# Performance work log

Hardware: AMD Instinct MI355X
Metric: run time of the kernel (lower is better)

## Reference

```python
import jax, jax.numpy as jnp
import numpy as np

D_MODEL = 1024
NUM_HEADS = 16
THETA = 10000.0
NEG = -1000000.0  # masked_fill value used by the torch code


def _rope(x, token_positions, theta):
    # x: [B, H, S, d_head]; token_positions: [S] int
    d_k = x.shape[-1]
    half = d_k // 2
    j = jnp.arange(half, dtype=jnp.float32)
    inv_freq = theta ** (-(2.0 * j) / d_k)                      # [half]
    ang = token_positions.astype(jnp.float32)[:, None] * inv_freq  # [S, half]
    cos = jnp.cos(ang)
    sin = jnp.sin(ang)
    xp = x.reshape(x.shape[:-1] + (half, 2))  # adjacent pairs (pc, 2)
    x0, x1 = xp[..., 0], xp[..., 1]
    o0 = x0 * cos - x1 * sin
    o1 = x0 * sin + x1 * cos
    out = jnp.stack([o0, o1], axis=-1)
    return out.reshape(x.shape)


def setup_inputs() -> dict:
    key = jax.random.key(0)
    k0, k1, k2 = jax.random.split(key, 3)
    B, S, D = 2, 2048, D_MODEL
    std = (2.0 / (D + D)) ** 0.5
    X = jax.random.normal(k0, (B, S, D), dtype=jnp.float32)
    QKV_weights = jax.random.normal(k1, (3 * D, D), dtype=jnp.float32) * std
    O_weights = jax.random.normal(k2, (D, D), dtype=jnp.float32) * std
    token_positions = jnp.arange(S, dtype=jnp.int32)
    return {"X": X, "token_positions": token_positions,
            "QKV_weights": QKV_weights, "O_weights": O_weights}


def reference(X, token_positions, QKV_weights, O_weights):
    B, S, D = X.shape
    H = NUM_HEADS
    dh = D // H
    qkv = jnp.einsum('od,bsd->bso', QKV_weights, X)  # [B, S, 3D]
    Q, K, V = jnp.split(qkv, 3, axis=-1)

    def split_heads(t):
        return t.reshape(B, S, H, dh).transpose(0, 2, 1, 3)  # [B,H,S,dh]

    Q, K, V = split_heads(Q), split_heads(K), split_heads(V)
    Q = _rope(Q, token_positions, THETA)
    K = _rope(K, token_positions, THETA)

    scores = (jnp.einsum('bhqd,bhkd->bhqk', Q, K) / jnp.sqrt(jnp.float32(dh))).astype(jnp.float32)
    causal = jnp.tril(jnp.ones((S, S), dtype=bool))
    scores = jnp.where(causal, scores, NEG)
    probs = jax.nn.softmax(scores, axis=-1)
    attn = jnp.einsum('bhqk,bhkd->bhqd', probs, V.astype(jnp.float32)).astype(Q.dtype)
    attn = attn.transpose(0, 2, 1, 3).reshape(B, S, D)
    return jnp.einsum('od,bsd->bso', O_weights, attn)
```

## Files before the change

### kernel.cpp

```cpp
#include <hip/hip_runtime.h>
#include <math.h>

#define S_LEN 2048

using bf16x8  = __attribute__((ext_vector_type(8))) short;
using shortx4 = __attribute__((ext_vector_type(4))) short;
using f32x4   = __attribute__((ext_vector_type(4))) float;
using uintx4  = __attribute__((ext_vector_type(4))) unsigned;
using uintx2  = __attribute__((ext_vector_type(2))) unsigned;

static __device__ __forceinline__ short f2bf(float f) {
  unsigned u = __float_as_uint(f);
  u += 0x7fffu + ((u >> 16) & 1u);
  return (short)(u >> 16);
}

#if __has_builtin(__builtin_amdgcn_cvt_pk_bf16_f32)
using bf16x2_t = __attribute__((ext_vector_type(2))) __bf16;
static __device__ __forceinline__ unsigned pkbf(float a, float b) {
  bf16x2_t v = __builtin_amdgcn_cvt_pk_bf16_f32(a, b);
  return __builtin_bit_cast(unsigned, v);
}
#else
static __device__ __forceinline__ unsigned pkbf(float a, float b) {
  return (unsigned)(unsigned short)f2bf(a) | ((unsigned)(unsigned short)f2bf(b) << 16);
}
#endif

#define GLD_LDS16(gptr, lptr)                                                  \
  __builtin_amdgcn_global_load_lds(                                            \
      (__attribute__((address_space(1))) void*)(gptr),                         \
      (__attribute__((address_space(3))) void*)(lptr), 16, 0, 0)

#define EXP2_SHIFT 20.0f

static __device__ __forceinline__ f32x4 exp2s4(f32x4 a) {
  return (f32x4){__builtin_amdgcn_exp2f(a[0] - EXP2_SHIFT),
                 __builtin_amdgcn_exp2f(a[1] - EXP2_SHIFT),
                 __builtin_amdgcn_exp2f(a[2] - EXP2_SHIFT),
                 __builtin_amdgcn_exp2f(a[3] - EXP2_SHIFT)};
}

static __device__ __forceinline__ int sigma64(int k) {
  return (k & 0x20) | ((k & 0x0C) << 1) | ((k & 0x10) >> 2) | (k & 3);
}

__global__ __launch_bounds__(256) void init_kernel(const float* __restrict__ X,
                                                   const float* __restrict__ W1,
                                                   const float* __restrict__ W2,
                                                   const int* __restrict__ tok,
                                                   short* __restrict__ Xb,
                                                   short* __restrict__ W1b,
                                                   short* __restrict__ W2b,
                                                   float2* __restrict__ table) {
  if (blockIdx.x < 4096) {
    size_t idx = (size_t)(blockIdx.x * 256 + threadIdx.x) * 8;
    const float* src;
    short* dst;
    size_t off;
    if (idx < 4194304) { src = X; dst = Xb; off = idx; }
    else if (idx < 4194304 + 3145728) { src = W1; dst = W1b; off = idx - 4194304; }
    else { src = W2; dst = W2b; off = idx - (4194304 + 3145728); }
    float4 a = *(const float4*)(src + off);
    float4 b = *(const float4*)(src + off + 4);
    bf16x8 o = {f2bf(a.x), f2bf(a.y), f2bf(a.z), f2bf(a.w),
                f2bf(b.x), f2bf(b.y), f2bf(b.z), f2bf(b.w)};
    *(bf16x8*)(dst + off) = o;
  } else {
    int i = (blockIdx.x - 4096) * 256 + threadIdx.x;
    int s = i >> 5, j = i & 31;
    double pos = (double)tok[s];
    double ang = pos * pow(10000.0, -(double)j / 32.0);
    table[i] = make_float2((float)cos(ang), (float)sin(ang));
  }
}

template <int BM, typename OutT, int EPI>
__global__ __launch_bounds__(256) void gemm_ll(const short* __restrict__ A,
                                               const short* __restrict__ B,
                                               OutT* __restrict__ C,
                                               const float2* __restrict__ tab,
                                               short* __restrict__ Qb,
                                               short* __restrict__ Kb,
                                               short* __restrict__ VT,
                                               int M, int N, int K) {
  constexpr int MI = BM / 32;
  constexpr int AI = BM / 64;
  __shared__ short As[BM * 32];
  __shared__ short Bs[128 * 32];
  const int tid  = threadIdx.x;
  const int lane = tid & 63;
  const int wv   = tid >> 6;
  const int wm   = (wv >> 1) * (BM / 2);
  const int wn   = (wv & 1) * 64;
  const int m16  = lane & 15;
  const int q4   = lane >> 4;

  const int nwg = gridDim.x * gridDim.y;
  int bid = blockIdx.y * gridDim.x + blockIdx.x;
  bid = (bid & 7) * (nwg >> 3) + (bid >> 3);
  const int rowBase = (bid / gridDim.x) * BM;
  const int colBase = (bid % gridDim.x) * 128;

  const int lrow = lane >> 2;
  const int lchk = (lane & 3) ^ ((lane >> 3) & 3);
  const int fsw  = (q4 ^ ((m16 >> 1) & 3)) * 8;

  f32x4 acc[MI][4];
#pragma unroll
  for (int i = 0; i < MI; ++i)
#pragma unroll
    for (int j = 0; j < 4; ++j) acc[i][j] = (f32x4){0.f, 0.f, 0.f, 0.f};

  const short* Agl = A + (size_t)rowBase * K;
  const short* Bgl = B + (size_t)colBase * K;

  for (int kk = 0; kk < K; kk += 32) {
#pragma unroll
    for (int i = 0; i < AI; ++i) {
      const int r0 = (wv * AI + i) * 16;
      GLD_LDS16(Agl + (size_t)(r0 + lrow) * K + kk + lchk * 8, &As[r0 * 32]);
    }
#pragma unroll
    for (int i = 0; i < 2; ++i) {
      const int r0 = (wv * 2 + i) * 16;
      GLD_LDS16(Bgl + (size_t)(r0 + lrow) * K + kk + lchk * 8, &Bs[r0 * 32]);
    }
    __syncthreads();

    bf16x8 af[MI], bfv[4];
#pragma unroll
    for (int mi = 0; mi < MI; ++mi)
      af[mi] = *(const bf16x8*)&As[(wm + mi * 16 + m16) * 32 + fsw];
#pragma unroll
    for (int ni = 0; ni < 4; ++ni)
      bfv[ni] = *(const bf16x8*)&Bs[(wn + ni * 16 + m16) * 32 + fsw];
#pragma unroll
    for (int mi = 0; mi < MI; ++mi)
#pragma unroll
      for (int ni = 0; ni < 4; ++ni)
        acc[mi][ni] = __builtin_amdgcn_mfma_f32_16x16x32_bf16(af[mi], bfv[ni], acc[mi][ni], 0, 0, 0);
    __syncthreads();
  }

  if constexpr (EPI == 0) {
#pragma unroll
    for (int mi = 0; mi < MI; ++mi)
#pragma unroll
      for (int ni = 0; ni < 4; ++ni) {
        const int rbase = rowBase + wm + mi * 16 + q4 * 4;
        const int cidx  = colBase + wn + ni * 16 + m16;
#pragma unroll
        for (int r = 0; r < 4; ++r) {
          float v = acc[mi][ni][r];
          if constexpr (sizeof(OutT) == 2)
            C[(size_t)(rbase + r) * N + cidx] = (OutT)f2bf(v);
          else
            C[(size_t)(rbase + r) * N + cidx] = (OutT)v;
        }
      }
  } else {
    const int sect = colBase >> 10;
#pragma unroll
    for (int mi = 0; mi < MI; ++mi)
#pragma unroll
      for (int ni = 0; ni < 4; ++ni) {
        const int col = colBase + wn + ni * 16 + m16;
        const int rb  = rowBase + wm + mi * 16 + q4 * 4;
        if (sect == 2) {
          const int hd = col - 2048;
          const int h = hd >> 6, d = hd & 63;
          const int b = rb >> 11, s0 = rb & (S_LEN - 1);
          shortx4 pk4 = {f2bf(acc[mi][ni][0]), f2bf(acc[mi][ni][1]),
                         f2bf(acc[mi][ni][2]), f2bf(acc[mi][ni][3])};
          *(shortx4*)(VT + ((size_t)((b * 16 + h) * 64 + d)) * S_LEN +
                      (s0 & ~63) + sigma64(s0 & 63)) = pk4;
        } else {
          const int cc = col & 1023;
          const int h = cc >> 6, d = cc & 63, j = d >> 1;
          const float sgn = (m16 & 1) ? 1.f : -1.f;
          short* dstp = (sect == 0) ? Qb : Kb;
          const float scl = (sect == 0) ? (0.125f * 1.44269504f) : 1.f;
#pragma unroll
          for (int r = 0; r < 4; ++r) {
            const int row = rb + r;
            const int s = row & (S_LEN - 1), bidx = row >> 11;
            float2 cs = tab[s * 32 + j];
            float self = acc[mi][ni][r];
            float part = __shfl_xor(self, 1);
            float o = (self * cs.x + sgn * part * cs.y) * scl;
            dstp[((size_t)((bidx * 16 + h) * S_LEN + s)) * 64 + d] = f2bf(o);
          }
        }
      }
  }
}

__global__ __launch_bounds__(256, 2) void attn_mfma(const short* __restrict__ Qb,
                                                    const short* __restrict__ Kb,
                                                    const short* __restrict__ VT,
                                                    short* __restrict__ attnb) {
  __shared__ __align__(16) short Smem[9216];
  short* Ks = Smem;
  short* Vs = Smem + 64 * 72;
  const int tid  = threadIdx.x;
  const int lane = tid & 63;
  const int w    = tid >> 6;
  const int m16  = lane & 15;
  const int q4   = lane >> 4;
  const int bh   = blockIdx.x;
  const int jtx  = blockIdx.y;
  const int jt   = (jtx < 8) ? (15 - jtx) : (jtx - 8);
  const int b    = bh >> 4, h = bh & 15;
  const short* Qh = Qb + (size_t)bh * S_LEN * 64;
  const short* Kh = Kb + (size_t)bh * S_LEN * 64;
  const short* Vh = VT + (size_t)bh * 64 * S_LEN;

  const int srow = tid >> 3;
  const int seg  = tid & 7;

  const bf16x8 ones = {16256, 16256, 16256, 16256, 16256, 16256, 16256, 16256};

  const int q0 = jt * 128;
  const int ktiles = 2 * jt + 2;

  bf16x8 qf[2][2];
#pragma unroll
  for (int n = 0; n < 2; ++n)
#pragma unroll
    for (int ks = 0; ks < 2; ++ks)
      qf[n][ks] = *(const bf16x8*)(Qh + (size_t)(q0 + w * 32 + n * 16 + m16) * 64 + ks * 32 + q4 * 8);

  f32x4 O[2][4], Lacc[2];
#pragma unroll
  for (int n = 0; n < 2; ++n) {
    Lacc[n] = (f32x4){0.f, 0.f, 0.f, 0.f};
#pragma unroll
    for (int c = 0; c < 4; ++c) O[n][c] = (f32x4){0.f, 0.f, 0.f, 0.f};
  }

  bf16x8 kst[2], vst[2];
#pragma unroll
  for (int i = 0; i < 2; ++i) {
    kst[i] = *(const bf16x8*)(Kh + (size_t)(i * 32 + srow) * 64 + seg * 8);
    vst[i] = *(const bf16x8*)(Vh + (size_t)(i * 32 + srow) * S_LEN + seg * 8);
  }

  for (int t = 0; t < ktiles; ++t) {
#pragma unroll
    for (int i = 0; i < 2; ++i) {
      *(bf16x8*)&Ks[(i * 32 + srow) * 72 + seg * 8] = kst[i];
      *(bf16x8*)&Vs[(i * 32 + srow) * 72 + seg * 8] = vst[i];
    }
    __syncthreads();

    if (t + 1 < ktiles) {
#pragma unroll
      for (int i = 0; i < 2; ++i) {
        kst[i] = *(const bf16x8*)(Kh + (size_t)((t + 1) * 64 + i * 32 + srow) * 64 + seg * 8);
        vst[i] = *(const bf16x8*)(Vh + (size_t)(i * 32 + srow) * S_LEN + (t + 1) * 64 + seg * 8);
      }
    }

    f32x4 sc[2][4];
#pragma unroll
    for (int n = 0; n < 2; ++n)
#pragma unroll
      for (int c = 0; c < 4; ++c) sc[n][c] = (f32x4){0.f, 0.f, 0.f, 0.f};
#pragma unroll
    for (int ks = 0; ks < 2; ++ks) {
#pragma unroll
      for (int c = 0; c < 4; ++c) {
        bf16x8 kf = *(const bf16x8*)&Ks[(c * 16 + m16) * 72 + ks * 32 + q4 * 8];
#pragma unroll
        for (int n = 0; n < 2; ++n)
          sc[n][c] = __builtin_amdgcn_mfma_f32_16x16x32_bf16(kf, qf[n][ks], sc[n][c], 0, 0, 0);
      }
    }

    if (t >= ktiles - 2) {
#pragma unroll
      for (int n = 0; n < 2; ++n)
#pragma unroll
        for (int c = 0; c < 4; ++c) {
          const int qg = q0 + w * 32 + n * 16 + m16;
#pragma unroll
          for (int rr = 0; rr < 4; ++rr) {
            const int kg = t * 64 + c * 16 + q4 * 4 + rr;
            if (kg > qg) sc[n][c][rr] = -1e30f;
          }
        }
    }

    bf16x8 pb[2][2];
#pragma unroll
    for (int n = 0; n < 2; ++n) {
#pragma unroll
      for (int c = 0; c < 4; ++c) sc[n][c] = exp2s4(sc[n][c]);
      uintx4 u0 = {pkbf(sc[n][0][0], sc[n][0][1]), pkbf(sc[n][0][2], sc[n][0][3]),
                   pkbf(sc[n][1][0], sc[n][1][1]), pkbf(sc[n][1][2], sc[n][1][3])};
      uintx4 u1 = {pkbf(sc[n][2][0], sc[n][2][1]), pkbf(sc[n][2][2], sc[n][2][3]),
                   pkbf(sc[n][3][0], sc[n][3][1]), pkbf(sc[n][3][2], sc[n][3][3])};
      pb[n][0] = __builtin_bit_cast(bf16x8, u0);
      pb[n][1] = __builtin_bit_cast(bf16x8, u1);
    }

#pragma unroll
    for (int ch = 0; ch < 2; ++ch) {
#pragma unroll
      for (int c2 = 0; c2 < 4; ++c2) {
        bf16x8 va = *(const bf16x8*)&Vs[(c2 * 16 + m16) * 72 + ch * 32 + q4 * 8];
#pragma unroll
        for (int n = 0; n < 2; ++n)
          O[n][c2] = __builtin_amdgcn_mfma_f32_16x16x32_bf16(va, pb[n][ch], O[n][c2], 0, 0, 0);
      }
#pragma unroll
      for (int n = 0; n < 2; ++n)
        Lacc[n] = __builtin_amdgcn_mfma_f32_16x16x32_bf16(ones, pb[n][ch], Lacc[n], 0, 0, 0);
    }
    __syncthreads();
  }

#pragma unroll
  for (int n = 0; n < 2; ++n) {
    const float inv = __frcp_rn(Lacc[n][0]);
#pragma unroll
    for (int c2 = 0; c2 < 4; ++c2) {
      uintx2 uo = {pkbf(O[n][c2][0] * inv, O[n][c2][1] * inv),
                   pkbf(O[n][c2][2] * inv, O[n][c2][3] * inv)};
      *(shortx4*)&Smem[(w * 32 + n * 16 + m16) * 72 + c2 * 16 + q4 * 4] =
          __builtin_bit_cast(shortx4, uo);
    }
  }
  __syncthreads();
  {
    const int row = tid >> 1, hf = tid & 1;
    const short* src = &Smem[row * 72 + hf * 32];
    short* dst = attnb + (size_t)(b * S_LEN + q0 + row) * 1024 + h * 64 + hf * 32;
    ((bf16x8*)dst)[0] = ((const bf16x8*)src)[0];
    ((bf16x8*)dst)[1] = ((const bf16x8*)src)[1];
    ((bf16x8*)dst)[2] = ((const bf16x8*)src)[2];
    ((bf16x8*)dst)[3] = ((const bf16x8*)src)[3];
  }
}

extern "C" void kernel_launch(void* const* d_in, const int* in_sizes, int n_in,
                              void* d_out, int out_size, void* d_ws, size_t ws_size,
                              hipStream_t stream) {
  const float* X    = (const float*)d_in[0];
  const int*   tok  = (const int*)d_in[1];
  const float* Wqkv = (const float*)d_in[2];
  const float* Wo   = (const float*)d_in[3];
  float* out = (float*)d_out;

  char* w = (char*)d_ws;
  float2* table = (float2*)w;
  short*  Qb    = (short*)(w + 524288);
  short*  Kb    = Qb + 4194304;
  short*  VTt   = Kb + 4194304;
  short*  Xb    = VTt + 2 * 4194304;
  short*  Wqkvb = Xb + 4194304;
  short*  Wob   = Wqkvb + 3145728;
  short*  attnb = Wob + 1048576;

  hipLaunchKernelGGL(init_kernel, dim3(4352), dim3(256), 0, stream,
                     X, Wqkv, Wo, tok, Xb, Wqkvb, Wob, table);
  hipLaunchKernelGGL((gemm_ll<128, short, 1>), dim3(24, 32), dim3(256), 0, stream,
                     Xb, Wqkvb, (short*)nullptr, table, Qb, Kb, VTt, 4096, 3072, 1024);
  hipLaunchKernelGGL(attn_mfma, dim3(32, 16), dim3(256), 0, stream,
                     Qb, Kb, VTt, attnb);
  hipLaunchKernelGGL((gemm_ll<128, float, 0>), dim3(8, 32), dim3(256), 0, stream,
                     attnb, Wob, out, (const float2*)nullptr,
                     (short*)nullptr, (short*)nullptr, (short*)nullptr,
                     4096, 1024, 1024);
}
```

Measured before the change: 184.3 us.

## Widen GEMM K-tile to 64 with new LDS swizzle; add MFMA setprio in attention

The projection GEMM now stages 64-wide K slices into LDS instead of 32, using an 8-row XOR swizzle for loads and fragment reads, and runs two MFMA k-steps per barrier pair. This halves the number of barrier rounds and global-to-LDS issue phases per output tile, at the cost of doubling LDS use per block. Separately, the attention kernel raises wave priority around its MFMA sections so matrix work is favoured over other waves' memory and exp work.

```diff
diff --git a/kernel.cpp b/kernel.cpp
--- a/kernel.cpp
+++ b/kernel.cpp
@@ -85,9 +85,9 @@
                                                short* __restrict__ VT,
                                                int M, int N, int K) {
   constexpr int MI = BM / 32;
-  constexpr int AI = BM / 64;
-  __shared__ short As[BM * 32];
-  __shared__ short Bs[128 * 32];
+  constexpr int AG = BM / 32;
+  __shared__ short As[BM * 64];
+  __shared__ short Bs[128 * 64];
   const int tid  = threadIdx.x;
   const int lane = tid & 63;
   const int wv   = tid >> 6;
@@ -102,9 +102,10 @@
   const int rowBase = (bid / gridDim.x) * BM;
   const int colBase = (bid % gridDim.x) * 128;
 
-  const int lrow = lane >> 2;
-  const int lchk = (lane & 3) ^ ((lane >> 3) & 3);
-  const int fsw  = (q4 ^ ((m16 >> 1) & 3)) * 8;
+  const int r8 = lane >> 3;
+  const int sl = lane & 7;
+  const int ssw = (sl ^ r8) * 8;
+  const int fx  = (m16 & 7);
 
   f32x4 acc[MI][4];
 #pragma unroll
@@ -115,31 +116,35 @@
   const short* Agl = A + (size_t)rowBase * K;
   const short* Bgl = B + (size_t)colBase * K;
 
-  for (int kk = 0; kk < K; kk += 32) {
-#pragma unroll
-    for (int i = 0; i < AI; ++i) {
-      const int r0 = (wv * AI + i) * 16;
-      GLD_LDS16(Agl + (size_t)(r0 + lrow) * K + kk + lchk * 8, &As[r0 * 32]);
-    }
-#pragma unroll
-    for (int i = 0; i < 2; ++i) {
-      const int r0 = (wv * 2 + i) * 16;
-      GLD_LDS16(Bgl + (size_t)(r0 + lrow) * K + kk + lchk * 8, &Bs[r0 * 32]);
+  for (int kk = 0; kk < K; kk += 64) {
+#pragma unroll
+    for (int i = 0; i < AG; ++i) {
+      const int g = wv * AG + i;
+      GLD_LDS16(Agl + (size_t)(g * 8 + r8) * K + kk + ssw, &As[g * 512]);
+    }
+#pragma unroll
+    for (int i = 0; i < 4; ++i) {
+      const int g = wv * 4 + i;
+      GLD_LDS16(Bgl + (size_t)(g * 8 + r8) * K + kk + ssw, &Bs[g * 512]);
     }
     __syncthreads();
 
-    bf16x8 af[MI], bfv[4];
-#pragma unroll
-    for (int mi = 0; mi < MI; ++mi)
-      af[mi] = *(const bf16x8*)&As[(wm + mi * 16 + m16) * 32 + fsw];
-#pragma unroll
-    for (int ni = 0; ni < 4; ++ni)
-      bfv[ni] = *(const bf16x8*)&Bs[(wn + ni * 16 + m16) * 32 + fsw];
-#pragma unroll
-    for (int mi = 0; mi < MI; ++mi)
+#pragma unroll
+    for (int ks = 0; ks < 2; ++ks) {
+      const int fo = ((ks * 4 + q4) ^ fx) * 8;
+      bf16x8 af[MI], bfv[4];
 #pragma unroll
       for (int ni = 0; ni < 4; ++ni)
-        acc[mi][ni] = __builtin_amdgcn_mfma_f32_16x16x32_bf16(af[mi], bfv[ni], acc[mi][ni], 0, 0, 0);
+        bfv[ni] = *(const bf16x8*)&Bs[(wn + ni * 16 + m16) * 64 + fo];
+#pragma unroll
+      for (int mi = 0; mi < MI; ++mi)
+        af[mi] = *(const bf16x8*)&As[(wm + mi * 16 + m16) * 64 + fo];
+#pragma unroll
+      for (int mi = 0; mi < MI; ++mi)
+#pragma unroll
+        for (int ni = 0; ni < 4; ++ni)
+          acc[mi][ni] = __builtin_amdgcn_mfma_f32_16x16x32_bf16(af[mi], bfv[ni], acc[mi][ni], 0, 0, 0);
+    }
     __syncthreads();
   }
 
@@ -267,6 +272,7 @@
     for (int n = 0; n < 2; ++n)
 #pragma unroll
       for (int c = 0; c < 4; ++c) sc[n][c] = (f32x4){0.f, 0.f, 0.f, 0.f};
+    __builtin_amdgcn_s_setprio(1);
 #pragma unroll
     for (int ks = 0; ks < 2; ++ks) {
 #pragma unroll
@@ -277,6 +283,7 @@
           sc[n][c] = __builtin_amdgcn_mfma_f32_16x16x32_bf16(kf, qf[n][ks], sc[n][c], 0, 0, 0);
       }
     }
+    __builtin_amdgcn_s_setprio(0);
 
     if (t >= ktiles - 2) {
 #pragma unroll
@@ -305,6 +312,7 @@
       pb[n][1] = __builtin_bit_cast(bf16x8, u1);
     }
 
+    __builtin_amdgcn_s_setprio(1);
 #pragma unroll
     for (int ch = 0; ch < 2; ++ch) {
 #pragma unroll
@@ -318,6 +326,7 @@
       for (int n = 0; n < 2; ++n)
         Lacc[n] = __builtin_amdgcn_mfma_f32_16x16x32_bf16(ones, pb[n][ch], Lacc[n], 0, 0, 0);
     }
+    __builtin_amdgcn_s_setprio(0);
     __syncthreads();
   }
 
```

Measured after the change: 189.8 us. 3.0% more time.

## Stage full-K weight panel in LDS and stream A fragments from global

Applied to the files above, without the earlier changes.

Replaces the k-looped tiled GEMM with a kernel that loads a whole 64-column by 1024-K weight panel (128 KB) into swizzled LDS once. Each wave then reads its A fragments directly from global memory with double-buffered registers, so the main loop has no block barriers. This removes per-k-step synchronisation and LDS staging of A, at the cost of very high LDS use (one block per CU) and uncached-in-LDS A reads that depend on L2/L1 reuse. Separately, the attention kernel raises wave priority around its MFMA sections.

```diff
diff --git a/kernel.cpp b/kernel.cpp
--- a/kernel.cpp
+++ b/kernel.cpp
@@ -75,98 +75,99 @@
   }
 }
 
-template <int BM, typename OutT, int EPI>
-__global__ __launch_bounds__(256) void gemm_ll(const short* __restrict__ A,
-                                               const short* __restrict__ B,
-                                               OutT* __restrict__ C,
+template <int EPI>
+__global__ __launch_bounds__(512) void gemm_bs(const short* __restrict__ A,
+                                               const short* __restrict__ Bw,
+                                               float* __restrict__ C,
                                                const float2* __restrict__ tab,
                                                short* __restrict__ Qb,
                                                short* __restrict__ Kb,
-                                               short* __restrict__ VT,
-                                               int M, int N, int K) {
-  constexpr int MI = BM / 32;
-  constexpr int AI = BM / 64;
-  __shared__ short As[BM * 32];
-  __shared__ short Bs[128 * 32];
+                                               short* __restrict__ VT) {
+  __shared__ short Bs[65536];
   const int tid  = threadIdx.x;
   const int lane = tid & 63;
   const int wv   = tid >> 6;
-  const int wm   = (wv >> 1) * (BM / 2);
-  const int wn   = (wv & 1) * 64;
   const int m16  = lane & 15;
   const int q4   = lane >> 4;
 
-  const int nwg = gridDim.x * gridDim.y;
-  int bid = blockIdx.y * gridDim.x + blockIdx.x;
-  bid = (bid & 7) * (nwg >> 3) + (bid >> 3);
-  const int rowBase = (bid / gridDim.x) * BM;
-  const int colBase = (bid % gridDim.x) * 128;
-
-  const int lrow = lane >> 2;
-  const int lchk = (lane & 3) ^ ((lane >> 3) & 3);
-  const int fsw  = (q4 ^ ((m16 >> 1) & 3)) * 8;
-
-  f32x4 acc[MI][4];
-#pragma unroll
-  for (int i = 0; i < MI; ++i)
+  const int bid = blockIdx.x;
+  const int mtg = bid & 15;
+  const int ntb = bid >> 4;
+
+  {
+    const short* Bgl = Bw + (size_t)ntb * 64 * 1024;
+    const int u = tid >> 7;
+    const int slot = tid & 127;
+#pragma unroll
+    for (int j = 0; j < 16; ++j) {
+      const int r = j * 4 + u;
+      const int gs = slot ^ (r & 7);
+      GLD_LDS16(Bgl + (size_t)r * 1024 + gs * 8, &Bs[j * 4096 + tid * 8]);
+    }
+  }
+  __syncthreads();
+
+  const int mtb = mtg * 256 + wv * 32;
+  const short* Aw = A + (size_t)(mtb + m16) * 1024 + q4 * 8;
+  const int bsw = (m16 & 7);
+
+  f32x4 acc[2][4];
+#pragma unroll
+  for (int i = 0; i < 2; ++i)
 #pragma unroll
     for (int j = 0; j < 4; ++j) acc[i][j] = (f32x4){0.f, 0.f, 0.f, 0.f};
 
-  const short* Agl = A + (size_t)rowBase * K;
-  const short* Bgl = B + (size_t)colBase * K;
-
-  for (int kk = 0; kk < K; kk += 32) {
-#pragma unroll
-    for (int i = 0; i < AI; ++i) {
-      const int r0 = (wv * AI + i) * 16;
-      GLD_LDS16(Agl + (size_t)(r0 + lrow) * K + kk + lchk * 8, &As[r0 * 32]);
-    }
-#pragma unroll
-    for (int i = 0; i < 2; ++i) {
-      const int r0 = (wv * 2 + i) * 16;
-      GLD_LDS16(Bgl + (size_t)(r0 + lrow) * K + kk + lchk * 8, &Bs[r0 * 32]);
-    }
-    __syncthreads();
-
-    bf16x8 af[MI], bfv[4];
-#pragma unroll
-    for (int mi = 0; mi < MI; ++mi)
-      af[mi] = *(const bf16x8*)&As[(wm + mi * 16 + m16) * 32 + fsw];
-#pragma unroll
-    for (int ni = 0; ni < 4; ++ni)
-      bfv[ni] = *(const bf16x8*)&Bs[(wn + ni * 16 + m16) * 32 + fsw];
-#pragma unroll
-    for (int mi = 0; mi < MI; ++mi)
-#pragma unroll
-      for (int ni = 0; ni < 4; ++ni)
-        acc[mi][ni] = __builtin_amdgcn_mfma_f32_16x16x32_bf16(af[mi], bfv[ni], acc[mi][ni], 0, 0, 0);
-    __syncthreads();
-  }
+#define LDA(t, mi) (*(const bf16x8*)(Aw + (size_t)(mi) * 16384 + (size_t)(t) * 32))
+#define STEP(t, aX)                                                            \
+  do {                                                                         \
+    bf16x8 bfv[4];                                                             \
+    _Pragma("unroll")                                                          \
+    for (int ni = 0; ni < 4; ++ni)                                             \
+      bfv[ni] = *(const bf16x8*)&Bs[(ni * 16 + m16) * 1024 +                   \
+                                    (((t) * 4 + q4) ^ bsw) * 8];               \
+    _Pragma("unroll")                                                          \
+    for (int mi = 0; mi < 2; ++mi)                                             \
+      _Pragma("unroll")                                                        \
+      for (int ni = 0; ni < 4; ++ni)                                           \
+        acc[mi][ni] = __builtin_amdgcn_mfma_f32_16x16x32_bf16(                 \
+            aX[mi], bfv[ni], acc[mi][ni], 0, 0, 0);                            \
+  } while (0)
+
+  bf16x8 aE[2], aO[2];
+#pragma unroll
+  for (int mi = 0; mi < 2; ++mi) aE[mi] = LDA(0, mi);
+  for (int t = 0; t < 32; t += 2) {
+#pragma unroll
+    for (int mi = 0; mi < 2; ++mi) aO[mi] = LDA(t + 1, mi);
+    STEP(t, aE);
+    if (t + 2 < 32) {
+#pragma unroll
+      for (int mi = 0; mi < 2; ++mi) aE[mi] = LDA(t + 2, mi);
+    }
+    STEP(t + 1, aO);
+  }
+#undef LDA
+#undef STEP
 
   if constexpr (EPI == 0) {
 #pragma unroll
-    for (int mi = 0; mi < MI; ++mi)
+    for (int mi = 0; mi < 2; ++mi)
 #pragma unroll
       for (int ni = 0; ni < 4; ++ni) {
-        const int rbase = rowBase + wm + mi * 16 + q4 * 4;
-        const int cidx  = colBase + wn + ni * 16 + m16;
-#pragma unroll
-        for (int r = 0; r < 4; ++r) {
-          float v = acc[mi][ni][r];
-          if constexpr (sizeof(OutT) == 2)
-            C[(size_t)(rbase + r) * N + cidx] = (OutT)f2bf(v);
-          else
-            C[(size_t)(rbase + r) * N + cidx] = (OutT)v;
-        }
+        const int rbase = mtb + mi * 16 + q4 * 4;
+        const int cidx  = ntb * 64 + ni * 16 + m16;
+#pragma unroll
+        for (int r = 0; r < 4; ++r)
+          C[(size_t)(rbase + r) * 1024 + cidx] = acc[mi][ni][r];
       }
   } else {
-    const int sect = colBase >> 10;
-#pragma unroll
-    for (int mi = 0; mi < MI; ++mi)
+    const int sect = ntb >> 4;
+#pragma unroll
+    for (int mi = 0; mi < 2; ++mi)
 #pragma unroll
       for (int ni = 0; ni < 4; ++ni) {
-        const int col = colBase + wn + ni * 16 + m16;
-        const int rb  = rowBase + wm + mi * 16 + q4 * 4;
+        const int col = ntb * 64 + ni * 16 + m16;
+        const int rb  = mtb + mi * 16 + q4 * 4;
         if (sect == 2) {
           const int hd = col - 2048;
           const int h = hd >> 6, d = hd & 63;
@@ -267,6 +268,7 @@
     for (int n = 0; n < 2; ++n)
 #pragma unroll
       for (int c = 0; c < 4; ++c) sc[n][c] = (f32x4){0.f, 0.f, 0.f, 0.f};
+    __builtin_amdgcn_s_setprio(1);
 #pragma unroll
     for (int ks = 0; ks < 2; ++ks) {
 #pragma unroll
@@ -277,6 +279,7 @@
           sc[n][c] = __builtin_amdgcn_mfma_f32_16x16x32_bf16(kf, qf[n][ks], sc[n][c], 0, 0, 0);
       }
     }
+    __builtin_amdgcn_s_setprio(0);
 
     if (t >= ktiles - 2) {
 #pragma unroll
@@ -305,6 +308,7 @@
       pb[n][1] = __builtin_bit_cast(bf16x8, u1);
     }
 
+    __builtin_amdgcn_s_setprio(1);
 #pragma unroll
     for (int ch = 0; ch < 2; ++ch) {
 #pragma unroll
@@ -318,6 +322,7 @@
       for (int n = 0; n < 2; ++n)
         Lacc[n] = __builtin_amdgcn_mfma_f32_16x16x32_bf16(ones, pb[n][ch], Lacc[n], 0, 0, 0);
     }
+    __builtin_amdgcn_s_setprio(0);
     __syncthreads();
   }
 
@@ -365,12 +370,11 @@
 
   hipLaunchKernelGGL(init_kernel, dim3(4352), dim3(256), 0, stream,
                      X, Wqkv, Wo, tok, Xb, Wqkvb, Wob, table);
-  hipLaunchKernelGGL((gemm_ll<128, short, 1>), dim3(24, 32), dim3(256), 0, stream,
-                     Xb, Wqkvb, (short*)nullptr, table, Qb, Kb, VTt, 4096, 3072, 1024);
+  hipLaunchKernelGGL((gemm_bs<1>), dim3(768), dim3(512), 0, stream,
+                     Xb, Wqkvb, (float*)nullptr, table, Qb, Kb, VTt);
   hipLaunchKernelGGL(attn_mfma, dim3(32, 16), dim3(256), 0, stream,
                      Qb, Kb, VTt, attnb);
-  hipLaunchKernelGGL((gemm_ll<128, float, 0>), dim3(8, 32), dim3(256), 0, stream,
+  hipLaunchKernelGGL((gemm_bs<0>), dim3(256), dim3(512), 0, stream,
                      attnb, Wob, out, (const float2*)nullptr,
-                     (short*)nullptr, (short*)nullptr, (short*)nullptr,
-                     4096, 1024, 1024);
-}
+                     (short*)nullptr, (short*)nullptr, (short*)nullptr);
+}
```

Measured after the change: 202.6 us. +9.9%, slower.
